# Kernel optimization log

Hardware: AMD Instinct MI355X
Metric: run time of the kernel (lower is better)

Reference implementation:

```python
import jax, jax.numpy as jnp
import numpy as np

B, R, N, D = 8, 5, 1024, 512  # batch, relations, utterances per dialogue, d_model
LN_EPS = 1e-5


def setup_inputs() -> dict:
    key = jax.random.key(0)
    k1, k2, k3 = jax.random.split(key, 3)
    h = jax.random.normal(k1, (B, N, D), dtype=jnp.float32)
    # Binary adjacency: adj[b, r, v, u] = 1 means u sends a message to v under relation r.
    adj = (jax.random.uniform(k2, (B, R, N, N)) < 0.5).astype(jnp.float32)
    # Relation 0 is the self-loop relation (identity), as in build_adjacency.
    adj = adj.at[:, 0].set(jnp.broadcast_to(jnp.eye(N, dtype=jnp.float32), (B, N, N)))
    # Per-relation Linear (bias=False) weights, torch convention: y = x @ W_r.T, W_r: (D, D)
    W = jax.random.normal(k3, (R, D, D), dtype=jnp.float32) * 0.02
    gamma = jnp.ones((D,), dtype=jnp.float32)
    beta = jnp.zeros((D,), dtype=jnp.float32)
    return {"h": h, "adj": adj, "W": W, "gamma": gamma, "beta": beta}


def reference(h, adj, W, gamma, beta):
    # Degree-normalize each relation's adjacency (row-normalized mean aggregation).
    deg = jnp.clip(jnp.sum(adj, axis=-1, keepdims=True), 1.0)  # (B,R,N,1)
    A = adj / deg
    # Mean aggregation per relation: (B,R,N,N) @ (B,N,D) -> (B,R,N,D)
    msg = jnp.einsum('brvu,bud->brvd', A, h)
    # Per-relation linear (x @ W_r.T) and sum over relations: (B,N,D)
    agg = jnp.einsum('brvd,red->bve', msg, W)
    # Dropout is identity in eval mode; ReLU, residual, LayerNorm.
    out = jax.nn.relu(agg) + h
    mu = jnp.mean(out, axis=-1, keepdims=True)
    xc = out - mu
    var = jnp.mean(xc * xc, axis=-1, keepdims=True)
    return xc / jnp.sqrt(var + LN_EPS) * gamma + beta
```

## Files before the change

kernel.cpp:

```cpp
#include <hip/hip_runtime.h>
#include <stdint.h>

#define Bd 8
#define Rr 5
#define Nn 1024
#define Dd 512
#define KK (Rr*Dd)

typedef __attribute__((ext_vector_type(8))) short bf16x8;
typedef __attribute__((ext_vector_type(4))) float f32x4;
typedef unsigned short u16;
typedef unsigned int u32;

__device__ __forceinline__ u16 f2bf(float x){
  union { float f; unsigned u; } v; v.f = x;
  unsigned r = v.u + 0x7FFFu + ((v.u >> 16) & 1u);
  return (u16)(r >> 16);
}

__device__ __forceinline__ void gll16(const void* g, void* l){
  __builtin_amdgcn_global_load_lds(
      (const __attribute__((address_space(1))) void*)g,
      (__attribute__((address_space(3))) void*)l, 16, 0, 0);
}

__global__ __launch_bounds__(256) void k_prep(
    const float* __restrict__ h, const float* __restrict__ W,
    u16* __restrict__ hTp, u16* __restrict__ Wt2, u16* __restrict__ msg){
  __shared__ float t32[32][65];
  const int tid = threadIdx.x;
  const int g = blockIdx.x;
  if (g < 2048){
    const int ut  = g & 31;
    const int dtg = (g >> 5) & 7;
    const int b   = g >> 8;
    const float* hb = h + ((size_t)b*Nn + (size_t)ut*32)*Dd + dtg*64;
    #pragma unroll
    for (int j=0;j<8;j++){
      int e = j*256 + tid;
      int ul = e >> 6, dl = e & 63;
      t32[ul][dl] = hb[(size_t)ul*Dd + dl];
    }
    __syncthreads();
    u16* ob = hTp + (size_t)b*Dd*Nn;
    #pragma unroll
    for (int j=0;j<8;j++){
      int e = j*256 + tid;
      int dtl = e >> 9;
      int rem = e & 511;
      int dr = rem >> 5, uu = rem & 31;
      int dt = dtg*4 + dtl;
      ob[((size_t)ut*32 + dt)*512 + rem] = f2bf(t32[uu][dtl*16 + dr]);
    }
  } else if (g < 3328){
    int idx = (g - 2048)*1024 + tid*4;
    int e = idx / KK;
    int k = idx % KK;
    int ri = (k < 2048) ? (1 + (k >> 9)) : 0;
    int d = k & 511;
    f32x4 w = *(const f32x4*)(W + (((size_t)ri*Dd + e)*Dd + d));
    u16 o[4] = { f2bf(w.x), f2bf(w.y), f2bf(w.z), f2bf(w.w) };
    *(uint2*)(Wt2 + idx) = *(uint2*)o;
  } else {
    int q = g - 3328;
    int row = q*4 + (tid >> 6);
    int d0 = (tid & 63)*8;
    f32x4 a = *(const f32x4*)(h + (size_t)row*Dd + d0);
    f32x4 c = *(const f32x4*)(h + (size_t)row*Dd + d0 + 4);
    bf16x8 pk;
    pk[0]=(short)f2bf(a.x); pk[1]=(short)f2bf(a.y);
    pk[2]=(short)f2bf(a.z); pk[3]=(short)f2bf(a.w);
    pk[4]=(short)f2bf(c.x); pk[5]=(short)f2bf(c.y);
    pk[6]=(short)f2bf(c.z); pk[7]=(short)f2bf(c.w);
    *(bf16x8*)(msg + (size_t)row*KK + 2048 + d0) = pk;
  }
}

__global__ __launch_bounds__(512,2) void k_msg(
    const float* __restrict__ adj, const u16* __restrict__ hTp,
    u16* __restrict__ msg){
  __shared__ __align__(16) u16 sA[2][4][32*64];
  __shared__ float sT[16*516];
  __shared__ float sDeg[4][32];

  const int tid  = threadIdx.x;
  const int lane = tid & 63;
  const int wave = tid >> 6;
  const int b  = blockIdx.x & 7;
  const int vt = blockIdx.x >> 3;
  const int v0 = vt * 32;
  const int t0 = blockIdx.x & 15;
  const float* adjb = adj + (((size_t)b*Rr + 1)*Nn + v0)*Nn;
  const u16* hTpb = hTp + (size_t)b*Dd*Nn;

  const int srow = tid >> 4;
  const int sc   = tid & 15;
  const size_t aoff = (size_t)srow*Nn + sc*4;
  const int wslot = sc ^ ((srow & 7) << 1);

  float deg[4] = {0.f,0.f,0.f,0.f};
  f32x4 aregA[4], aregB[4];
  f32x4 acc[4][2][4];
  #pragma unroll
  for (int ri=0;ri<4;ri++)
    #pragma unroll
    for (int m=0;m<2;m++)
      #pragma unroll
      for (int n=0;n<4;n++) acc[ri][m][n] = (f32x4){0.f,0.f,0.f,0.f};

  const int rlo = lane & 15, ch = lane >> 4;
  const int boff = rlo*32 + ch*8;

  #define TT(x) (((x) + t0) & 15)

  #define AISSUE(DST, T) do {                                                 \
    _Pragma("unroll")                                                         \
    for (int ri=0;ri<4;ri++)                                                  \
      DST[ri] = *(const f32x4*)(adjb + (size_t)ri*Nn*Nn + (size_t)(T)*64 + aoff); \
  } while(0)

  #define PACK(SRC, BUFI) do {                                                \
    _Pragma("unroll")                                                         \
    for (int ri=0;ri<4;ri++){                                                 \
      f32x4 p = SRC[ri];                                                      \
      deg[ri] += p.x+p.y+p.z+p.w;                                             \
      uint2 pk;                           \
      pk.x = (__float_as_uint(p.x)>>16) | (__float_as_uint(p.y) & 0xFFFF0000u);\
      pk.y = (__float_as_uint(p.z)>>16) | (__float_as_uint(p.w) & 0xFFFF0000u);\
      *(uint2*)((char*)sA[BUFI][ri] + srow*128 + wslot*8) = pk;               \
    }                                                                         \
  } while(0)

  #define LOADB(DST, T) do {                                                  \
    _Pragma("unroll")                                                         \
    for (int kk=0;kk<2;kk++){                                                 \
      const u16* bp = hTpb + ((((size_t)((T)*2+kk))*32 + (wave<<2))<<9) + boff;\
      _Pragma("unroll")                                                       \
      for (int n=0;n<4;n++)                                                   \
        DST[kk][n] = *(const bf16x8*)(bp + ((size_t)n<<9));                   \
    }                                                                         \
  } while(0)

  #define MSTEP(BFR, BUFI) do {                                               \
    const char* abase = (const char*)sA[BUFI];                                \
    _Pragma("unroll")                                                         \
    for (int kk=0;kk<2;kk++){                                                 \
      _Pragma("unroll")                                                       \
      for (int ri=0;ri<4;ri++){                                               \
        bf16x8 af[2];                                                         \
        _Pragma("unroll")                                                     \
        for (int m=0;m<2;m++){                                                \
          const int row = m*16 + rlo;                                         \
          af[m] = *(const bf16x8*)(abase + ri*4096 + row*128                  \
                    + (((kk*8 + ch*2) ^ ((row&7)<<1))<<3));                   \
        }                                                                     \
        _Pragma("unroll")                                                     \
        for (int m=0;m<2;m++)                                                 \
          _Pragma("unroll")                                                   \
          for (int n=0;n<4;n++)                                               \
            acc[ri][m][n] = __builtin_amdgcn_mfma_f32_16x16x32_bf16(          \
                af[m], BFR[kk][n], acc[ri][m][n], 0, 0, 0);                   \
      }                                                                       \
    }                                                                         \
  } while(0)

  #define STEP_BARRIER() do {                                                 \
    asm volatile("s_waitcnt lgkmcnt(0)" ::: "memory");                        \
    __builtin_amdgcn_sched_barrier(0);                                        \
    __builtin_amdgcn_s_barrier();                                             \
    __builtin_amdgcn_sched_barrier(0);                                        \
  } while(0)

  AISSUE(aregA, TT(0));
  PACK(aregA, 0);
  __syncthreads();
  AISSUE(aregA, TT(1));

  for (int t = 0; t < 14; t += 2){
    {
      bf16x8 bfr[2][4];
      LOADB(bfr, TT(t));
      AISSUE(aregB, TT(t+2));
      PACK(aregA, 1);
      MSTEP(bfr, 0);
      STEP_BARRIER();
    }
    {
      bf16x8 bfr[2][4];
      LOADB(bfr, TT(t+1));
      AISSUE(aregA, TT(t+3));
      PACK(aregB, 0);
      MSTEP(bfr, 1);
      STEP_BARRIER();
    }
  }
  {
    bf16x8 bfr[2][4];
    LOADB(bfr, TT(14));
    PACK(aregA, 1);
    MSTEP(bfr, 0);
    STEP_BARRIER();
  }
  {
    bf16x8 bfr[2][4];
    LOADB(bfr, TT(15));
    MSTEP(bfr, 1);
  }
  #undef TT
  #undef AISSUE
  #undef PACK
  #undef LOADB
  #undef MSTEP
  #undef STEP_BARRIER

  #pragma unroll
  for (int ri=0;ri<4;ri++){
    float d = deg[ri];
    d += __shfl_xor(d, 1); d += __shfl_xor(d, 2);
    d += __shfl_xor(d, 4); d += __shfl_xor(d, 8);
    if (sc == 0) sDeg[ri][srow] = d;
  }
  __syncthreads();

  u16* mb = msg + ((size_t)b*Nn + v0)*KK;
  #pragma unroll
  for (int ri=0;ri<4;ri++){
    #pragma unroll
    for (int hh=0;hh<2;hh++){
      #pragma unroll
      for (int reg=0;reg<4;reg++){
        const int rl = ch*4 + reg;
        const float inv = 1.0f / fmaxf(sDeg[ri][hh*16 + rl], 1.0f);
        #pragma unroll
        for (int n=0;n<4;n++){
          const int col = (wave<<6) + n*16 + rlo;
          const int colw = col ^ (((col>>5)&7)<<2);
          sT[rl*516 + colw] = acc[ri][hh][n][reg] * inv;
        }
      }
      __syncthreads();
      #pragma unroll
      for (int s=0;s<2;s++){
        const int rl = wave*2 + s;
        const int m5 = lane >> 2;
        const int e  = m5 & 7;
        const int j0 = (2*lane) & 7;
        f32x4 lo = *(const f32x4*)&sT[rl*516 + (m5<<5) + (((j0  ) ^ e)<<2)];
        f32x4 hi = *(const f32x4*)&sT[rl*516 + (m5<<5) + (((j0+1) ^ e)<<2)];
        bf16x8 pk;
        pk[0]=(short)f2bf(lo.x); pk[1]=(short)f2bf(lo.y);
        pk[2]=(short)f2bf(lo.z); pk[3]=(short)f2bf(lo.w);
        pk[4]=(short)f2bf(hi.x); pk[5]=(short)f2bf(hi.y);
        pk[6]=(short)f2bf(hi.z); pk[7]=(short)f2bf(hi.w);
        *(bf16x8*)(mb + (size_t)(hh*16 + rl)*KK + ri*512 + lane*8) = pk;
      }
      __syncthreads();
    }
  }
}

__global__ __launch_bounds__(512,4) void k_agg(
    const u16* __restrict__ msg, const u16* __restrict__ Wt,
    float* __restrict__ agg){
  __shared__ __align__(16) u16 sA[2][64*64];
  __shared__ __align__(16) u16 sB[2][128*64];
  const int tid = threadIdx.x;
  const int lane = tid & 63, wave = tid >> 6;
  const int wm = wave >> 2, wn = wave & 3;
  const int g = blockIdx.x;
  const int et = g >> 7;
  const int bv = g & 127;
  const int b  = bv >> 4;
  const int vt = bv & 15;
  const int v0 = vt*64, e0 = et*128;
  const u16* Ab = msg + ((size_t)b*Nn + v0)*KK;
  const u16* Bb = Wt + (size_t)e0*KK;

  f32x4 acc[2][2];
  #pragma unroll
  for (int m=0;m<2;m++)
    #pragma unroll
    for (int n=0;n<2;n++) acc[m][n] = (f32x4){0.f,0.f,0.f,0.f};

  #define STAGE(buf, kt) do {                                              \
    { int c = tid; int row_ = c>>3, chg = (c&7) ^ (row_&7);                \
      gll16(Ab + (size_t)row_*KK + (kt)*64 + chg*8,                        \
            (char*)sA[buf] + ((size_t)(wave<<6))*16); }                    \
    _Pragma("unroll")                                                      \
    for (int i=0;i<2;i++){                                                 \
      int c = i*512 + tid; int row_ = c>>3, chg = (c&7) ^ (row_&7);        \
      gll16(Bb + (size_t)row_*KK + (kt)*64 + chg*8,                        \
            (char*)sB[buf] + ((size_t)(i*512 + (wave<<6)))*16);            \
    }                                                                      \
  } while(0)

  STAGE(0, 0);
  __syncthreads();

  const int ch = lane >> 4, rlo = lane & 15;

  for (int kt = 0; kt < KK/64; ++kt){
    if (kt < KK/64 - 1) STAGE((kt+1)&1, kt+1);
    const char* a  = (const char*)sA[kt&1];
    const char* bb = (const char*)sB[kt&1];
    #pragma unroll
    for (int kk=0; kk<2; ++kk){
      bf16x8 af[2], bfx[2];
      #pragma unroll
      for (int m=0;m<2;m++){
        const int row = wm*32 + m*16 + rlo;
        af[m] = *(const bf16x8*)(a + row*128 + ((((kk<<2)+ch) ^ (row&7))<<4));
      }
      #pragma unroll
      for (int n=0;n<2;n++){
        const int row = wn*32 + n*16 + rlo;
        bfx[n] = *(const bf16x8*)(bb + row*128 + ((((kk<<2)+ch) ^ (row&7))<<4));
      }
      #pragma unroll
      for (int m=0;m<2;m++)
        #pragma unroll
        for (int n=0;n<2;n++)
          acc[m][n] = __builtin_amdgcn_mfma_f32_16x16x32_bf16(af[m], bfx[n], acc[m][n], 0, 0, 0);
    }
    __syncthreads();
  }
  #undef STAGE

  float* ob = agg + ((size_t)b*Nn + v0)*Dd + e0;
  #pragma unroll
  for (int m=0;m<2;m++)
    #pragma unroll
    for (int reg=0;reg<4;reg++){
      const int row = wm*32 + m*16 + ((lane>>4)<<2) + reg;
      #pragma unroll
      for (int n=0;n<2;n++){
        const int col = wn*32 + n*16 + (lane & 15);
        ob[(size_t)row*Dd + col] = acc[m][n][reg];
      }
    }
}

__global__ __launch_bounds__(256,4) void k_ln(
    const float* __restrict__ agg, const float* __restrict__ h,
    const float* __restrict__ gamma, const float* __restrict__ beta,
    float* __restrict__ out){
  const int row = blockIdx.x*4 + (threadIdx.x >> 6);
  const int lane = threadIdx.x & 63;
  const float* a  = agg + (size_t)row*Dd;
  const float* hh = h   + (size_t)row*Dd;
  float x[8];
  float sum = 0.f, sq = 0.f;
  #pragma unroll
  for (int q=0;q<2;q++){
    f32x4 av = *(const f32x4*)(a  + ((size_t)q*64+lane)*4);
    f32x4 hv = *(const f32x4*)(hh + ((size_t)q*64+lane)*4);
    #pragma unroll
    for (int k=0;k<4;k++){
      float v = fmaxf(av[k], 0.f) + hv[k];
      x[q*4+k] = v; sum += v; sq += v*v;
    }
  }
  #pragma unroll
  for (int off=32; off; off>>=1){
    sum += __shfl_xor(sum, off);
    sq  += __shfl_xor(sq,  off);
  }
  const float mu  = sum * (1.f/(float)Dd);
  const float var = sq * (1.f/(float)Dd) - mu*mu;
  const float rstd = rsqrtf(var + 1e-5f);
  float* o = out + (size_t)row*Dd;
  #pragma unroll
  for (int q=0;q<2;q++){
    f32x4 g  = *(const f32x4*)(gamma + ((size_t)q*64+lane)*4);
    f32x4 be = *(const f32x4*)(beta  + ((size_t)q*64+lane)*4);
    f32x4 ov;
    #pragma unroll
    for (int k=0;k<4;k++)
      ov[k] = (x[q*4+k] - mu) * rstd * g[k] + be[k];
    *(f32x4*)(o + ((size_t)q*64+lane)*4) = ov;
  }
}

extern "C" void kernel_launch(void* const* d_in, const int* in_sizes, int n_in,
                              void* d_out, int out_size, void* d_ws, size_t ws_size,
                              hipStream_t stream){
  const float* h     = (const float*)d_in[0];
  const float* adj   = (const float*)d_in[1];
  const float* W     = (const float*)d_in[2];
  const float* gamma = (const float*)d_in[3];
  const float* beta  = (const float*)d_in[4];
  float* out = (float*)d_out;
  char* ws = (char*)d_ws;

  u16*  hTp = (u16*)(ws);
  u16*  Wt2 = (u16*)(ws + 8388608);
  u16*  msg = (u16*)(ws + 11010048);
  float* agg = (float*)(ws + 52953088);

  k_prep<<<dim3(5376), dim3(256), 0, stream>>>(h, W, hTp, Wt2, msg);
  k_msg <<<dim3(Bd*32), dim3(512), 0, stream>>>(adj, hTp, msg);
  k_agg <<<dim3(Bd*(Nn/64)*(Dd/128)), dim3(512), 0, stream>>>(msg, Wt2, agg);
  k_ln  <<<dim3(Bd*Nn/4), dim3(256), 0, stream>>>(agg, h, gamma, beta, out);
}
```

Before: 96.03 us.

## Restructure adjacency-GEMM main loop into single-buffered register pipeline with sched fences

New measurement: 92.12 us (median of 3 runs). 4.1% less time.

```diff
diff --git a/kernel.cpp b/kernel.cpp
--- a/kernel.cpp
+++ b/kernel.cpp
@@ -99,7 +99,7 @@
   const int wslot = sc ^ ((srow & 7) << 1);
 
   float deg[4] = {0.f,0.f,0.f,0.f};
-  f32x4 aregA[4], aregB[4];
+  f32x4 areg[4];
   f32x4 acc[4][2][4];
   #pragma unroll
   for (int ri=0;ri<4;ri++)
@@ -113,16 +113,16 @@
 
   #define TT(x) (((x) + t0) & 15)
 
-  #define AISSUE(DST, T) do {                                                 \
+  #define AISSUE(T) do {                                                      \
     _Pragma("unroll")                                                         \
     for (int ri=0;ri<4;ri++)                                                  \
-      DST[ri] = *(const f32x4*)(adjb + (size_t)ri*Nn*Nn + (size_t)(T)*64 + aoff); \
-  } while(0)
-
-  #define PACK(SRC, BUFI) do {                                                \
+      areg[ri] = *(const f32x4*)(adjb + (size_t)ri*Nn*Nn + (size_t)(T)*64 + aoff); \
+  } while(0)
+
+  #define PACK(BUFI) do {                                                     \
     _Pragma("unroll")                                                         \
     for (int ri=0;ri<4;ri++){                                                 \
-      f32x4 p = SRC[ri];                                                      \
+      f32x4 p = areg[ri];                                                     \
       deg[ri] += p.x+p.y+p.z+p.w;                                             \
       uint2 pk;                           \
       pk.x = (__float_as_uint(p.x)>>16) | (__float_as_uint(p.y) & 0xFFFF0000u);\
@@ -131,17 +131,17 @@
     }                                                                         \
   } while(0)
 
-  #define LOADB(DST, T) do {                                                  \
+  #define LOADB(T) do {                                                      \
     _Pragma("unroll")                                                         \
     for (int kk=0;kk<2;kk++){                                                 \
       const u16* bp = hTpb + ((((size_t)((T)*2+kk))*32 + (wave<<2))<<9) + boff;\
       _Pragma("unroll")                                                       \
       for (int n=0;n<4;n++)                                                   \
-        DST[kk][n] = *(const bf16x8*)(bp + ((size_t)n<<9));                   \
+        bfr[kk][n] = *(const bf16x8*)(bp + ((size_t)n<<9));                   \
     }                                                                         \
   } while(0)
 
-  #define MSTEP(BFR, BUFI) do {                                               \
+  #define MSTEP(BUFI) do {                                                    \
     const char* abase = (const char*)sA[BUFI];                                \
     _Pragma("unroll")                                                         \
     for (int kk=0;kk<2;kk++){                                                 \
@@ -159,58 +159,46 @@
           _Pragma("unroll")                                                   \
           for (int n=0;n<4;n++)                                               \
             acc[ri][m][n] = __builtin_amdgcn_mfma_f32_16x16x32_bf16(          \
-                af[m], BFR[kk][n], acc[ri][m][n], 0, 0, 0);                   \
+                af[m], bfr[kk][n], acc[ri][m][n], 0, 0, 0);                   \
       }                                                                       \
     }                                                                         \
   } while(0)
 
+  #define FENCE() __builtin_amdgcn_sched_barrier(0)
   #define STEP_BARRIER() do {                                                 \
     asm volatile("s_waitcnt lgkmcnt(0)" ::: "memory");                        \
-    __builtin_amdgcn_sched_barrier(0);                                        \
+    FENCE();                                                                  \
     __builtin_amdgcn_s_barrier();                                             \
-    __builtin_amdgcn_sched_barrier(0);                                        \
-  } while(0)
-
-  AISSUE(aregA, TT(0));
-  PACK(aregA, 0);
+    FENCE();                                                                  \
+  } while(0)
+
+  bf16x8 bfr[2][4];
+
+  AISSUE(TT(0));
+  PACK(0);
   __syncthreads();
-  AISSUE(aregA, TT(1));
-
-  for (int t = 0; t < 14; t += 2){
-    {
-      bf16x8 bfr[2][4];
-      LOADB(bfr, TT(t));
-      AISSUE(aregB, TT(t+2));
-      PACK(aregA, 1);
-      MSTEP(bfr, 0);
-      STEP_BARRIER();
-    }
-    {
-      bf16x8 bfr[2][4];
-      LOADB(bfr, TT(t+1));
-      AISSUE(aregA, TT(t+3));
-      PACK(aregB, 0);
-      MSTEP(bfr, 1);
-      STEP_BARRIER();
-    }
-  }
-  {
-    bf16x8 bfr[2][4];
-    LOADB(bfr, TT(14));
-    PACK(aregA, 1);
-    MSTEP(bfr, 0);
+  LOADB(TT(0));
+  FENCE();
+  AISSUE(TT(1));
+  FENCE();
+
+  for (int t = 0; t < 15; ++t){
+    PACK((t+1)&1);
+    FENCE();
+    if (t < 14) AISSUE(TT(t+2));
+    FENCE();
+    MSTEP(t&1);
+    FENCE();
+    LOADB(TT(t+1));
     STEP_BARRIER();
   }
-  {
-    bf16x8 bfr[2][4];
-    LOADB(bfr, TT(15));
-    MSTEP(bfr, 1);
-  }
+  MSTEP(1);
   #undef TT
   #undef AISSUE
   #undef PACK
   #undef LOADB
   #undef MSTEP
+  #undef FENCE
   #undef STEP_BARRIER
 
   #pragma unroll
```
